# Optimization experiments

Measured on AMD Instinct MI355X. Metric: run time of the kernel, lower is better.

## Reference

```python
import jax, jax.numpy as jnp
import numpy as np

DIM = 768
HEADS = 12
HEAD_DIM = DIM // HEADS
SCALE = HEAD_DIM ** -0.5


def setup_inputs() -> dict:
    key = jax.random.key(0)
    ks = jax.random.split(key, 8)
    B, N, C = 8, 1024, DIM
    s = 0.02
    return {
        "x": jax.random.normal(ks[0], (B, N, C), jnp.float32),
        "y": jax.random.normal(ks[1], (B, N, C), jnp.float32),
        "x_qkv_w": jax.random.normal(ks[2], (3 * C, C), jnp.float32) * s,
        "y_qkv_w": jax.random.normal(ks[3], (3 * C, C), jnp.float32) * s,
        "x_proj_w": jax.random.normal(ks[4], (C, C), jnp.float32) * s,
        "x_proj_b": jnp.zeros((C,), jnp.float32),
        "y_proj_w": jax.random.normal(ks[5], (C, C), jnp.float32) * s,
        "y_proj_b": jnp.zeros((C,), jnp.float32),
    }


def _split_qkv(t, qkv_w):
    # t: [B,N,C] -> q,k,v each [B,H,N,D]
    B, N, C = t.shape
    qkv = t @ qkv_w.T                      # [B,N,3C]
    qkv = qkv.reshape(B, N, 3, HEADS, HEAD_DIM).transpose(2, 0, 3, 1, 4)
    return qkv[0], qkv[1], qkv[2]


def reference(x, y, x_qkv_w, y_qkv_w, x_proj_w, x_proj_b, y_proj_w, y_proj_b):
    B, N, C = x.shape
    x_q, x_k, x_v = _split_qkv(x, x_qkv_w)
    y_q, y_k, y_v = _split_qkv(y, y_qkv_w)

    # scores: [B,H,N,N]; dropout is identity (attn_drop=0)
    x_attn = jax.nn.softmax(jnp.einsum('bhnd,bhmd->bhnm', x_q * SCALE, x_k), axis=-1)
    y_attn = jax.nn.softmax(jnp.einsum('bhnd,bhmd->bhnm', y_q * SCALE, y_k), axis=-1)

    # swapped V aggregation: x-branch attends over y_v, y-branch over x_v
    x_out = jnp.einsum('bhnm,bhmd->bhnd', x_attn, y_v).transpose(0, 2, 1, 3).reshape(B, N, C)
    y_out = jnp.einsum('bhnm,bhmd->bhnd', y_attn, x_v).transpose(0, 2, 1, 3).reshape(B, N, C)

    x_out = x_out @ x_proj_w.T + x_proj_b
    y_out = y_out @ y_proj_w.T + y_proj_b
    return (x_out, y_out)
```

## Files before the change

kernel.cpp:

```cpp
#include <hip/hip_runtime.h>
#include <hip/hip_bf16.h>
#include <stdint.h>
#include <stddef.h>

typedef unsigned short u16;
typedef __attribute__((ext_vector_type(8))) short bf16x8;
typedef __attribute__((ext_vector_type(4))) short bf16x4;
typedef __attribute__((ext_vector_type(4))) float f32x4;
typedef __attribute__((ext_vector_type(16))) float f32x16;
typedef __attribute__((ext_vector_type(4))) unsigned short u16x4;

#define MFMA_BF16 __builtin_amdgcn_mfma_f32_16x16x32_bf16
#define MFMA32    __builtin_amdgcn_mfma_f32_32x32x16_bf16

#if defined(__has_builtin)
#if __has_builtin(__builtin_amdgcn_exp2f)
#define EXP2F(x) __builtin_amdgcn_exp2f(x)
#endif
#endif
#ifndef EXP2F
#define EXP2F(x) __expf((x) * 0.6931471805599453f)
#endif

__device__ __forceinline__ void pl32swap(unsigned& a, unsigned& b) {
#if defined(__has_builtin) && __has_builtin(__builtin_amdgcn_permlane32_swap)
  typedef int v2i __attribute__((ext_vector_type(2)));
  v2i r = __builtin_amdgcn_permlane32_swap((int)a, (int)b, false, false);
  a = (unsigned)r.x;
  b = (unsigned)r.y;
#else
  asm volatile("v_permlane32_swap_b32 %0, %1" : "+v"(a), "+v"(b));
#endif
}

#define BAR_FULL asm volatile("s_waitcnt vmcnt(0)\n\ts_barrier" ::: "memory")
#define BAR_CNT4 asm volatile("s_waitcnt vmcnt(4)\n\ts_barrier" ::: "memory")

#define QSCALE 0.18033688011112042f

__device__ __forceinline__ u16 f2b(float x) {
  uint32_t u = __builtin_bit_cast(uint32_t, x);
  return (u16)((u + 0x7fffu + ((u >> 16) & 1u)) >> 16);
}

__device__ __forceinline__ unsigned pk2(float a, float b) {
  union { __hip_bfloat162 h; unsigned u; } c;
  c.h = __float22bfloat162_rn(make_float2(a, b));
  return c.u;
}

__device__ __forceinline__ void async16(const void* g, void* l) {
  __builtin_amdgcn_global_load_lds((const __attribute__((address_space(1))) void*)g,
                                   (__attribute__((address_space(3))) void*)l, 16, 0, 0);
}

__global__ void cvt_all(const float* __restrict__ x, const float* __restrict__ y,
                        const float* __restrict__ xqw, const float* __restrict__ yqw,
                        const float* __restrict__ xpw, const float* __restrict__ ypw,
                        u16* __restrict__ dst) {
  long i = ((long)blockIdx.x * 256 + threadIdx.x) * 4;
  const float* src;
  long off;
  if (i < 6291456)       { src = x;   off = 0; }
  else if (i < 12582912) { src = y;   off = 6291456; }
  else if (i < 14352384) { src = xqw; off = 12582912; }
  else if (i < 16121856) { src = yqw; off = 14352384; }
  else if (i < 16711680) { src = xpw; off = 16121856; }
  else                   { src = ypw; off = 16711680; }
  float4 v = *(const float4*)(src + (i - off));
  u16x4 o = { f2b(v.x), f2b(v.y), f2b(v.z), f2b(v.w) };
  *(u16x4*)(dst + i) = o;
}

__global__ __launch_bounds__(256, 2)
void qkv_gemm(const u16* __restrict__ Xb, const u16* __restrict__ Yb,
              const u16* __restrict__ Wx, const u16* __restrict__ Wy,
              u16* __restrict__ Qx, u16* __restrict__ Kx, u16* __restrict__ Vtx,
              u16* __restrict__ Qy, u16* __restrict__ Ky, u16* __restrict__ Vty) {
  __shared__ alignas(16) char smem[65536];
  const int br = blockIdx.z;
  const u16* A = br ? Yb : Xb;
  const u16* W = br ? Wy : Wx;
  u16* Qd = br ? Qy : Qx;
  u16* Kd = br ? Ky : Kx;
  u16* Vd = br ? Vty : Vtx;
  const int m0 = blockIdx.x * 128;
  const int j0 = blockIdx.y * 128;
  const int tid = threadIdx.x;
  const int wave = tid >> 6, lane = tid & 63;
  const int quad = lane >> 4, l16 = lane & 15;
  const int wm = wave >> 1, wn = wave & 1;
  const int srow = wave * 32 + (lane >> 3);
  const int scol = (((lane & 7) ^ ((lane >> 3) & 7)) * 8);
  const int l7 = l16 & 7;

  auto stage = [&](int k0, int p) {
#pragma unroll
    for (int c = 0; c < 4; ++c) {
      async16(A + (size_t)(m0 + srow + c * 8) * 768 + k0 + scol,
              smem + p * 16384 + wave * 4096 + c * 1024);
      async16(W + (size_t)(j0 + srow + c * 8) * 768 + k0 + scol,
              smem + 32768 + p * 16384 + wave * 4096 + c * 1024);
    }
  };

  f32x4 acc[4][4] = {};
  stage(0, 0);

  for (int kt = 0; kt < 12; ++kt) {
    const int p = kt & 1;
    BAR_FULL;
    if (kt < 11) stage((kt + 1) * 64, p ^ 1);
    const u16* Ap = (const u16*)smem + p * 8192;
    const u16* Bp = (const u16*)smem + 16384 + p * 8192;
#pragma unroll
    for (int kc = 0; kc < 2; ++kc) {
      bf16x8 af[4], bfr[4];
#pragma unroll
      for (int t = 0; t < 4; ++t) {
        af[t]  = *(const bf16x8*)&Ap[(wm * 64 + t * 16 + l16) * 64 + (((kc * 4 + quad) ^ l7) * 8)];
        bfr[t] = *(const bf16x8*)&Bp[(wn * 64 + t * 16 + l16) * 64 + (((kc * 4 + quad) ^ l7) * 8)];
      }
#pragma unroll
      for (int mt = 0; mt < 4; ++mt)
#pragma unroll
        for (int nt = 0; nt < 4; ++nt)
          acc[mt][nt] = MFMA_BF16(af[mt], bfr[nt], acc[mt][nt], 0, 0, 0);
    }
  }

  __syncthreads();
  u16* Ts = (u16*)smem;
  const int s3 = j0 / 768;

  if (s3 == 2) {
#pragma unroll
    for (int mt = 0; mt < 4; ++mt)
#pragma unroll
      for (int nt = 0; nt < 4; ++nt) {
        const int j = wn * 64 + nt * 16 + l16;
        const int mb = wm * 64 + mt * 16 + quad * 4;
        u16x4 pk = { f2b(acc[mt][nt][0]), f2b(acc[mt][nt][1]),
                     f2b(acc[mt][nt][2]), f2b(acc[mt][nt][3]) };
        *(u16x4*)&Ts[j * 136 + mb] = pk;
      }
    __syncthreads();
#pragma unroll
    for (int rt = 0; rt < 8; ++rt) {
      const int j = wave * 32 + rt * 4 + (lane >> 4);
      const int mo = (lane & 15) * 8;
      bf16x8 v = *(const bf16x8*)&Ts[j * 136 + mo];
      const int jr = j0 + j - 1536;
      const int h = jr >> 6, d = jr & 63;
      const int gm = m0 + mo;
      const int b = gm >> 10, n = gm & 1023;
      *(bf16x8*)&Vd[((size_t)(b * 12 + h) * 64 + d) * 1024 + n] = v;
    }
  } else {
    const float qs = s3 ? 1.0f : QSCALE;
#pragma unroll
    for (int mt = 0; mt < 4; ++mt)
#pragma unroll
      for (int nt = 0; nt < 4; ++nt) {
        const int j = wn * 64 + nt * 16 + l16;
#pragma unroll
        for (int r = 0; r < 4; ++r) {
          const int m = wm * 64 + mt * 16 + quad * 4 + r;
          Ts[m * 136 + j] = f2b(acc[mt][nt][r] * qs);
        }
      }
    __syncthreads();
    u16* Dd = s3 ? Kd : Qd;
#pragma unroll
    for (int rt = 0; rt < 8; ++rt) {
      const int m = wave * 32 + rt * 4 + (lane >> 4);
      const int jh = (lane >> 3) & 1, jo = (lane & 7) * 8;
      bf16x8 v = *(const bf16x8*)&Ts[m * 136 + jh * 64 + jo];
      const int jr = j0 + jh * 64 + jo - s3 * 768;
      const int h = jr >> 6, d = jr & 63;
      const int gm = m0 + m;
      const int b = gm >> 10, n = gm & 1023;
      *(bf16x8*)&Dd[((size_t)(b * 12 + h) * 1024 + n) * 64 + d] = v;
    }
  }
}

__global__ __launch_bounds__(256, 3)
void attn_kernel(const u16* __restrict__ Qx, const u16* __restrict__ Kx, const u16* __restrict__ Vtx,
                 const u16* __restrict__ Qy, const u16* __restrict__ Ky, const u16* __restrict__ Vty,
                 u16* __restrict__ Ox, u16* __restrict__ Oy) {
  __shared__ alignas(16) u16 Ks[3][64 * 64];
  __shared__ alignas(16) u16 Vs[3][64 * 64];
  __shared__ float LSbuf[4][32];
  const int br = blockIdx.z;
  const u16* Q = br ? Qy : Qx;
  const u16* K = br ? Ky : Kx;
  const u16* V = br ? Vtx : Vty;
  u16* O = br ? Oy : Ox;
  const int bh = blockIdx.x;
  const int q0 = blockIdx.y * 128;
  const int tid = threadIdx.x;
  const int wave = tid >> 6, lane = tid & 63;
  const int l = lane & 31, hi = lane >> 5;
  const int l7 = lane & 7;
  const int r8 = (lane >> 3) & 7;
  const int sw = ((lane & 7) ^ r8) * 8;

  const u16* Qb = Q + (size_t)bh * 65536;
  const u16* Kb = K + (size_t)bh * 65536;
  const u16* Vb = V + (size_t)bh * 65536;

  const int krow = wave * 16 + r8;

  auto stage = [&](int kv0, int buf) {
#pragma unroll
    for (int c = 0; c < 2; ++c) {
      async16(Kb + (size_t)(kv0 + krow + c * 8) * 64 + sw, (char*)Ks[buf] + wave * 2048 + c * 1024);
      async16(Vb + (size_t)(krow + c * 8) * 1024 + kv0 + sw, (char*)Vs[buf] + wave * 2048 + c * 1024);
    }
  };

  stage(0, 0);
  bf16x8 qf[4];
#pragma unroll
  for (int dc = 0; dc < 4; ++dc)
    qf[dc] = *(const bf16x8*)(Qb + (size_t)(q0 + wave * 32 + l) * 64 + dc * 16 + hi * 8);
  stage(64, 1);

  f32x16 oacc[2] = {};
  float lsum = 0.f;

  union FrU { unsigned u[4]; bf16x8 v; };

  int pr = 0;
  for (int it = 0; it < 16; ++it) {
    if (it < 15) BAR_CNT4; else BAR_FULL;
    if (it < 14) {
      const int pw = (pr + 2 >= 3) ? pr - 1 : pr + 2;
      stage((it + 2) * 64, pw);
    }

    const u16* Kp = Ks[pr];
    const u16* Vp = Vs[pr];

#pragma unroll
    for (int s = 0; s < 2; ++s) {
      bf16x8 kf[4];
#pragma unroll
      for (int dc = 0; dc < 4; ++dc)
        kf[dc] = *(const bf16x8*)&Kp[(s * 32 + l) * 64 + (((dc * 2 + hi) ^ l7) * 8)];

      f32x16 st = {};
#pragma unroll
      for (int dc = 0; dc < 4; ++dc)
        st = MFMA32(kf[dc], qf[dc], st, 0, 0, 0);
      float pv[16];
#pragma unroll
      for (int r = 0; r < 16; ++r) pv[r] = EXP2F(st[r]);
      lsum += (((pv[0] + pv[1]) + (pv[2] + pv[3])) + ((pv[4] + pv[5]) + (pv[6] + pv[7])))
            + (((pv[8] + pv[9]) + (pv[10] + pv[11])) + ((pv[12] + pv[13]) + (pv[14] + pv[15])));
      unsigned P[8];
#pragma unroll
      for (int i = 0; i < 8; ++i) P[i] = pk2(pv[2 * i], pv[2 * i + 1]);
      FrU fragA[2];
#pragma unroll
      for (int f = 0; f < 2; ++f) {
        unsigned a0 = P[f * 4 + 0], b0 = P[f * 4 + 2];
        unsigned a1 = P[f * 4 + 1], b1 = P[f * 4 + 3];
        pl32swap(a0, b0);
        pl32swap(a1, b1);
        fragA[f].u[0] = a0;
        fragA[f].u[1] = a1;
        fragA[f].u[2] = b0;
        fragA[f].u[3] = b1;
      }
#pragma unroll
      for (int f = 0; f < 2; ++f)
#pragma unroll
        for (int dt = 0; dt < 2; ++dt) {
          bf16x8 vf = *(const bf16x8*)&Vp[(dt * 32 + l) * 64 + (((s * 4 + f * 2 + hi) ^ l7) * 8)];
          oacc[dt] = MFMA32(fragA[f].v, vf, oacc[dt], 0, 0, 0);
        }
    }
    pr = (pr == 2) ? 0 : pr + 1;
  }

  float* LS = LSbuf[wave];
  {
    float t0 = lsum + __shfl_xor(lsum, 32, 64);
    LS[l] = 1.0f / t0;
  }

  const int b = bh / 12, h = bh % 12;
#pragma unroll
  for (int r = 0; r < 16; ++r) {
    const int cr = (r & 3) + 8 * (r >> 2) + 4 * hi;
    const float iv = LS[cr];
    const int qrow = q0 + wave * 32 + cr;
    const size_t ob = ((size_t)(b * 1024 + qrow)) * 768 + h * 64;
#pragma unroll
    for (int dt = 0; dt < 2; ++dt)
      O[ob + dt * 32 + l] = f2b(oacc[dt][r] * iv);
  }
}

__global__ __launch_bounds__(256, 2)
void proj_gemm(const u16* __restrict__ Ox, const u16* __restrict__ Oy,
               const u16* __restrict__ Pxw, const u16* __restrict__ Pyw,
               const float* __restrict__ bx, const float* __restrict__ by,
               float* __restrict__ out) {
  __shared__ alignas(16) char smem[65536];
  const int br = blockIdx.z;
  const u16* A = br ? Oy : Ox;
  const u16* W = br ? Pyw : Pxw;
  const float* bias = br ? by : bx;
  float* op = out + (size_t)br * 6291456;
  const int m0 = blockIdx.x * 128;
  const int j0 = blockIdx.y * 128;
  const int tid = threadIdx.x;
  const int wave = tid >> 6, lane = tid & 63;
  const int quad = lane >> 4, l16 = lane & 15;
  const int wm = wave >> 1, wn = wave & 1;
  const int srow = wave * 32 + (lane >> 3);
  const int scol = (((lane & 7) ^ ((lane >> 3) & 7)) * 8);
  const int l7 = l16 & 7;

  auto stage = [&](int k0, int p) {
#pragma unroll
    for (int c = 0; c < 4; ++c) {
      async16(A + (size_t)(m0 + srow + c * 8) * 768 + k0 + scol,
              smem + p * 16384 + wave * 4096 + c * 1024);
      async16(W + (size_t)(j0 + srow + c * 8) * 768 + k0 + scol,
              smem + 32768 + p * 16384 + wave * 4096 + c * 1024);
    }
  };

  f32x4 acc[4][4] = {};
  stage(0, 0);

  for (int kt = 0; kt < 12; ++kt) {
    const int p = kt & 1;
    BAR_FULL;
    if (kt < 11) stage((kt + 1) * 64, p ^ 1);
    const u16* Ap = (const u16*)smem + p * 8192;
    const u16* Bp = (const u16*)smem + 16384 + p * 8192;
#pragma unroll
    for (int kc = 0; kc < 2; ++kc) {
      bf16x8 af[4], bfr[4];
#pragma unroll
      for (int t = 0; t < 4; ++t) {
        af[t]  = *(const bf16x8*)&Ap[(wm * 64 + t * 16 + l16) * 64 + (((kc * 4 + quad) ^ l7) * 8)];
        bfr[t] = *(const bf16x8*)&Bp[(wn * 64 + t * 16 + l16) * 64 + (((kc * 4 + quad) ^ l7) * 8)];
      }
#pragma unroll
      for (int mt = 0; mt < 4; ++mt)
#pragma unroll
        for (int nt = 0; nt < 4; ++nt)
          acc[mt][nt] = MFMA_BF16(af[mt], bfr[nt], acc[mt][nt], 0, 0, 0);
    }
  }

#pragma unroll
  for (int mt = 0; mt < 4; ++mt) {
#pragma unroll
    for (int nt = 0; nt < 4; ++nt) {
      const int j = j0 + wn * 64 + nt * 16 + l16;
      const float bj = bias[j];
#pragma unroll
      for (int r = 0; r < 4; ++r) {
        const int m = m0 + wm * 64 + mt * 16 + quad * 4 + r;
        op[(size_t)m * 768 + j] = acc[mt][nt][r] + bj;
      }
    }
  }
}

extern "C" void kernel_launch(void* const* d_in, const int* in_sizes, int n_in,
                              void* d_out, int out_size, void* d_ws, size_t ws_size,
                              hipStream_t stream) {
  (void)in_sizes; (void)n_in; (void)out_size; (void)ws_size;
  const float* x   = (const float*)d_in[0];
  const float* y   = (const float*)d_in[1];
  const float* xqw = (const float*)d_in[2];
  const float* yqw = (const float*)d_in[3];
  const float* xpw = (const float*)d_in[4];
  const float* xpb = (const float*)d_in[5];
  const float* ypw = (const float*)d_in[6];
  const float* ypb = (const float*)d_in[7];
  float* out = (float*)d_out;

  char* p = (char*)d_ws;
  u16* Xb  = (u16*)p; p += 12582912;
  u16* Yb  = (u16*)p; p += 12582912;
  u16* Wxb = (u16*)p; p += 3538944;
  u16* Wyb = (u16*)p; p += 3538944;
  u16* Pxb = (u16*)p; p += 1179648;
  u16* Pyb = (u16*)p; p += 1179648;
  u16* Qx  = (u16*)p; p += 12582912;
  u16* Kx  = (u16*)p; p += 12582912;
  u16* Vtx = (u16*)p; p += 12582912;
  u16* Qy  = (u16*)p; p += 12582912;
  u16* Ky  = (u16*)p; p += 12582912;
  u16* Vty = (u16*)p; p += 12582912;
  u16* Ox  = Xb;
  u16* Oy  = Yb;

  cvt_all<<<16896, 256, 0, stream>>>(x, y, xqw, yqw, xpw, ypw, Xb);

  qkv_gemm<<<dim3(64, 18, 2), 256, 0, stream>>>(Xb, Yb, Wxb, Wyb,
                                                Qx, Kx, Vtx, Qy, Ky, Vty);
  attn_kernel<<<dim3(96, 8, 2), 256, 0, stream>>>(Qx, Kx, Vtx, Qy, Ky, Vty, Ox, Oy);
  proj_gemm<<<dim3(64, 6, 2), 256, 0, stream>>>(Ox, Oy, Pxb, Pyb, xpb, ypb, out);
}
```

Measured before the change: 277.3 us.

## Use triple-buffered BK=32 pipeline in QKV and projection GEMMs

Both GEMM kernels change from a double-buffered K=64 tile loop to a triple-buffered K=32 loop that prefetches two stages ahead, using a partial-count barrier (BAR_CNT4) so one load group can stay in flight. LDS per block drops from 64KB to 48KB and launch bounds rise to 3 blocks per CU to raise occupancy. The smaller K tile doubles the number of barriers and loop iterations, and the third resident block raises register pressure. The new swizzle also has to stay bank-conflict free.

```diff
diff --git a/kernel.cpp b/kernel.cpp
--- a/kernel.cpp
+++ b/kernel.cpp
@@ -72,12 +72,12 @@
   *(u16x4*)(dst + i) = o;
 }
 
-__global__ __launch_bounds__(256, 2)
+__global__ __launch_bounds__(256, 3)
 void qkv_gemm(const u16* __restrict__ Xb, const u16* __restrict__ Yb,
               const u16* __restrict__ Wx, const u16* __restrict__ Wy,
               u16* __restrict__ Qx, u16* __restrict__ Kx, u16* __restrict__ Vtx,
               u16* __restrict__ Qy, u16* __restrict__ Ky, u16* __restrict__ Vty) {
-  __shared__ alignas(16) char smem[65536];
+  __shared__ alignas(16) char smem[49152];
   const int br = blockIdx.z;
   const u16* A = br ? Yb : Xb;
   const u16* W = br ? Wy : Wx;
@@ -90,43 +90,46 @@
   const int wave = tid >> 6, lane = tid & 63;
   const int quad = lane >> 4, l16 = lane & 15;
   const int wm = wave >> 1, wn = wave & 1;
-  const int srow = wave * 32 + (lane >> 3);
-  const int scol = (((lane & 7) ^ ((lane >> 3) & 7)) * 8);
-  const int l7 = l16 & 7;
-
-  auto stage = [&](int k0, int p) {
-#pragma unroll
-    for (int c = 0; c < 4; ++c) {
-      async16(A + (size_t)(m0 + srow + c * 8) * 768 + k0 + scol,
-              smem + p * 16384 + wave * 4096 + c * 1024);
-      async16(W + (size_t)(j0 + srow + c * 8) * 768 + k0 + scol,
-              smem + 32768 + p * 16384 + wave * 4096 + c * 1024);
+  const int srow = wave * 32 + (lane >> 2);
+  const int schunk = ((lane & 3) ^ ((lane >> 3) & 3)) * 8;
+  const int rsw = (l16 >> 1) & 3;
+
+  auto stage = [&](int kt, int buf) {
+    const int k0 = kt * 32;
+#pragma unroll
+    for (int c = 0; c < 2; ++c) {
+      async16(A + (size_t)(m0 + srow + c * 16) * 768 + k0 + schunk,
+              smem + buf * 16384 + wave * 2048 + c * 1024);
+      async16(W + (size_t)(j0 + srow + c * 16) * 768 + k0 + schunk,
+              smem + buf * 16384 + 8192 + wave * 2048 + c * 1024);
     }
   };
 
   f32x4 acc[4][4] = {};
   stage(0, 0);
-
-  for (int kt = 0; kt < 12; ++kt) {
-    const int p = kt & 1;
-    BAR_FULL;
-    if (kt < 11) stage((kt + 1) * 64, p ^ 1);
-    const u16* Ap = (const u16*)smem + p * 8192;
-    const u16* Bp = (const u16*)smem + 16384 + p * 8192;
-#pragma unroll
-    for (int kc = 0; kc < 2; ++kc) {
-      bf16x8 af[4], bfr[4];
-#pragma unroll
-      for (int t = 0; t < 4; ++t) {
-        af[t]  = *(const bf16x8*)&Ap[(wm * 64 + t * 16 + l16) * 64 + (((kc * 4 + quad) ^ l7) * 8)];
-        bfr[t] = *(const bf16x8*)&Bp[(wn * 64 + t * 16 + l16) * 64 + (((kc * 4 + quad) ^ l7) * 8)];
-      }
-#pragma unroll
-      for (int mt = 0; mt < 4; ++mt)
-#pragma unroll
-        for (int nt = 0; nt < 4; ++nt)
-          acc[mt][nt] = MFMA_BF16(af[mt], bfr[nt], acc[mt][nt], 0, 0, 0);
-    }
+  stage(1, 1);
+
+  int pr = 0;
+  for (int kt = 0; kt < 24; ++kt) {
+    if (kt < 23) BAR_CNT4; else BAR_FULL;
+    if (kt < 22) {
+      int pw = pr + 2; if (pw >= 3) pw -= 3;
+      stage(kt + 2, pw);
+    }
+    const u16* Ap = (const u16*)(smem + pr * 16384);
+    const u16* Bp = Ap + 4096;
+    bf16x8 af[4], bfr[4];
+#pragma unroll
+    for (int t = 0; t < 4; ++t) {
+      af[t]  = *(const bf16x8*)&Ap[(wm * 64 + t * 16 + l16) * 32 + ((quad ^ rsw) * 8)];
+      bfr[t] = *(const bf16x8*)&Bp[(wn * 64 + t * 16 + l16) * 32 + ((quad ^ rsw) * 8)];
+    }
+#pragma unroll
+    for (int mt = 0; mt < 4; ++mt)
+#pragma unroll
+      for (int nt = 0; nt < 4; ++nt)
+        acc[mt][nt] = MFMA_BF16(af[mt], bfr[nt], acc[mt][nt], 0, 0, 0);
+    pr = (pr == 2) ? 0 : pr + 1;
   }
 
   __syncthreads();
@@ -304,12 +307,12 @@
   }
 }
 
-__global__ __launch_bounds__(256, 2)
+__global__ __launch_bounds__(256, 3)
 void proj_gemm(const u16* __restrict__ Ox, const u16* __restrict__ Oy,
                const u16* __restrict__ Pxw, const u16* __restrict__ Pyw,
                const float* __restrict__ bx, const float* __restrict__ by,
                float* __restrict__ out) {
-  __shared__ alignas(16) char smem[65536];
+  __shared__ alignas(16) char smem[49152];
   const int br = blockIdx.z;
   const u16* A = br ? Oy : Ox;
   const u16* W = br ? Pyw : Pxw;
@@ -321,43 +324,46 @@
   const int wave = tid >> 6, lane = tid & 63;
   const int quad = lane >> 4, l16 = lane & 15;
   const int wm = wave >> 1, wn = wave & 1;
-  const int srow = wave * 32 + (lane >> 3);
-  const int scol = (((lane & 7) ^ ((lane >> 3) & 7)) * 8);
-  const int l7 = l16 & 7;
-
-  auto stage = [&](int k0, int p) {
-#pragma unroll
-    for (int c = 0; c < 4; ++c) {
-      async16(A + (size_t)(m0 + srow + c * 8) * 768 + k0 + scol,
-              smem + p * 16384 + wave * 4096 + c * 1024);
-      async16(W + (size_t)(j0 + srow + c * 8) * 768 + k0 + scol,
-              smem + 32768 + p * 16384 + wave * 4096 + c * 1024);
+  const int srow = wave * 32 + (lane >> 2);
+  const int schunk = ((lane & 3) ^ ((lane >> 3) & 3)) * 8;
+  const int rsw = (l16 >> 1) & 3;
+
+  auto stage = [&](int kt, int buf) {
+    const int k0 = kt * 32;
+#pragma unroll
+    for (int c = 0; c < 2; ++c) {
+      async16(A + (size_t)(m0 + srow + c * 16) * 768 + k0 + schunk,
+              smem + buf * 16384 + wave * 2048 + c * 1024);
+      async16(W + (size_t)(j0 + srow + c * 16) * 768 + k0 + schunk,
+              smem + buf * 16384 + 8192 + wave * 2048 + c * 1024);
     }
   };
 
   f32x4 acc[4][4] = {};
   stage(0, 0);
-
-  for (int kt = 0; kt < 12; ++kt) {
-    const int p = kt & 1;
-    BAR_FULL;
-    if (kt < 11) stage((kt + 1) * 64, p ^ 1);
-    const u16* Ap = (const u16*)smem + p * 8192;
-    const u16* Bp = (const u16*)smem + 16384 + p * 8192;
-#pragma unroll
-    for (int kc = 0; kc < 2; ++kc) {
-      bf16x8 af[4], bfr[4];
-#pragma unroll
-      for (int t = 0; t < 4; ++t) {
-        af[t]  = *(const bf16x8*)&Ap[(wm * 64 + t * 16 + l16) * 64 + (((kc * 4 + quad) ^ l7) * 8)];
-        bfr[t] = *(const bf16x8*)&Bp[(wn * 64 + t * 16 + l16) * 64 + (((kc * 4 + quad) ^ l7) * 8)];
-      }
-#pragma unroll
-      for (int mt = 0; mt < 4; ++mt)
-#pragma unroll
-        for (int nt = 0; nt < 4; ++nt)
-          acc[mt][nt] = MFMA_BF16(af[mt], bfr[nt], acc[mt][nt], 0, 0, 0);
-    }
+  stage(1, 1);
+
+  int pr = 0;
+  for (int kt = 0; kt < 24; ++kt) {
+    if (kt < 23) BAR_CNT4; else BAR_FULL;
+    if (kt < 22) {
+      int pw = pr + 2; if (pw >= 3) pw -= 3;
+      stage(kt + 2, pw);
+    }
+    const u16* Ap = (const u16*)(smem + pr * 16384);
+    const u16* Bp = Ap + 4096;
+    bf16x8 af[4], bfr[4];
+#pragma unroll
+    for (int t = 0; t < 4; ++t) {
+      af[t]  = *(const bf16x8*)&Ap[(wm * 64 + t * 16 + l16) * 32 + ((quad ^ rsw) * 8)];
+      bfr[t] = *(const bf16x8*)&Bp[(wn * 64 + t * 16 + l16) * 32 + ((quad ^ rsw) * 8)];
+    }
+#pragma unroll
+    for (int mt = 0; mt < 4; ++mt)
+#pragma unroll
+      for (int nt = 0; nt < 4; ++nt)
+        acc[mt][nt] = MFMA_BF16(af[mt], bfr[nt], acc[mt][nt], 0, 0, 0);
+    pr = (pr == 2) ? 0 : pr + 1;
   }
 
 #pragma unroll
```

After: 288.0 us. 3.9% more time.
